# Performance work log

Measured on AMD Instinct MI355X. Metric: run time of the kernel, lower is better.

Reference implementation:

```python
import jax, jax.numpy as jnp
import numpy as np

MARGIN = 1.0
EPS = 1e-12


def setup_inputs() -> dict:
    key = jax.random.key(0)
    k1, k2, k3 = jax.random.split(key, 3)
    B, C, D = 16384, 500, 512
    features = jax.random.normal(k1, (B, D), dtype=jnp.float32)
    prototypes = jax.random.normal(k2, (C, D), dtype=jnp.float32)
    labels = jax.random.randint(k3, (B,), 0, C, dtype=jnp.int64)
    return {"features": features, "prototypes": prototypes, "labels": labels}


def reference(features, prototypes, labels):
    # Pairwise L2 distances [B, C] via the expanded form (no [B,C,D] intermediate)
    f2 = jnp.sum(features * features, axis=-1, keepdims=True)   # [B, 1]
    p2 = jnp.sum(prototypes * prototypes, axis=-1)               # [C]
    sq = f2 + p2 - 2.0 * (features @ prototypes.T)               # [B, C]
    dists = jnp.sqrt(jnp.maximum(sq, EPS))                       # [B, C]

    B, C = dists.shape
    d_pos = jnp.take_along_axis(dists, labels[:, None], axis=1)[:, 0]  # [B]
    pos_mask = jax.nn.one_hot(labels, C, dtype=bool)             # [B, C]
    d_neg_min = jnp.min(jnp.where(pos_mask, jnp.inf, dists), axis=-1)  # [B]

    loss = jnp.mean(jax.nn.relu(d_pos - d_neg_min + MARGIN))
    return loss
```

## Files before the change

### kernel.cpp

```cpp
#include <hip/hip_runtime.h>
#include <stdint.h>
#include <stddef.h>

#define BB 16384
#define CC 500
#define DD 512
#define PADC 512
#define LMARGIN 1.0f
#define EPSQ 1e-12f
#define NK 16

typedef __attribute__((ext_vector_type(8))) _Float16 f16x8;
typedef __attribute__((ext_vector_type(4))) _Float16 f16x4;
typedef __attribute__((ext_vector_type(4))) float f32x4;

__global__ void prepP_kernel(const float* __restrict__ protos,
                             unsigned short* __restrict__ protoH,
                             float* __restrict__ p2,
                             float* __restrict__ out) {
  int c = blockIdx.x * 4 + (threadIdx.x >> 6);
  int lane = threadIdx.x & 63;
  if (c == 0 && lane == 0) out[0] = 0.f;
  f32x4 a0 = {0.f, 0.f, 0.f, 0.f}, a1 = a0;
  if (c < CC) {
    const float* src = protos + (size_t)c * DD + lane * 8;
    a0 = *(const f32x4*)src;
    a1 = *(const f32x4*)(src + 4);
  }
  f16x8 h;
  float s = 0.f;
#pragma unroll
  for (int u = 0; u < 4; ++u) {
    h[u] = (_Float16)a0[u];
    h[u + 4] = (_Float16)a1[u];
    s = fmaf(a0[u], a0[u], s);
    s = fmaf(a1[u], a1[u], s);
  }
  *(f16x8*)(protoH + (size_t)c * DD + lane * 8) = h;
#pragma unroll
  for (int d = 1; d < 64; d <<= 1) s += __shfl_xor(s, d, 64);
  if (lane == 0) p2[c] = s;
}

__launch_bounds__(512, 2)
__global__ void main_kernel(const float* __restrict__ feat,
                            const unsigned short* __restrict__ protoH,
                            const float* __restrict__ p2,
                            const int* __restrict__ labels,
                            float* __restrict__ f2ws,
                            float2* __restrict__ ws2) {
  __shared__ __align__(16) unsigned short Afull[NK][64][32];

  const int tid = threadIdx.x;
  const int w = tid >> 6;
  const int lane = tid & 63;
  const int lane16 = lane & 15;
  const int quad = lane >> 4;
  const int r0 = blockIdx.x * 64;

  const unsigned short* pb = protoH + (size_t)(w * 64 + lane16) * DD + quad * 8;

  f16x8 bcur[4], bnxt[4];
#pragma unroll
  for (int nt = 0; nt < 4; ++nt) bcur[nt] = *(const f16x8*)(pb + nt * 16 * DD);

  {
    const f32x4* fsrc = (const f32x4*)(feat + (size_t)r0 * DD);
    f32x4 a[NK];
#pragma unroll
    for (int i = 0; i < NK; ++i) a[i] = fsrc[w * 1024 + i * 64 + lane];

    float f2row[8] = {0.f, 0.f, 0.f, 0.f, 0.f, 0.f, 0.f, 0.f};
#pragma unroll
    for (int i = 0; i < NK; ++i) {
      const int row = w * 8 + (i >> 1);
      const int k = (i & 1) * 256 + lane * 4;
      f16x4 h;
      float s = 0.f;
#pragma unroll
      for (int u = 0; u < 4; ++u) {
        h[u] = (_Float16)a[i][u];
        s = fmaf(a[i][u], a[i][u], s);
      }
      *(f16x4*)(&Afull[k >> 5][row][k & 31]) = h;
#pragma unroll
      for (int d = 1; d < 64; d <<= 1) s += __shfl_xor(s, d, 64);
      f2row[i >> 1] += s;
    }
    if (lane == 0) {
#pragma unroll
      for (int j = 0; j < 8; ++j) f2ws[r0 + w * 8 + j] = f2row[j];
    }
  }

  f32x4 acc[4][4];
#pragma unroll
  for (int mt = 0; mt < 4; ++mt)
#pragma unroll
    for (int nt = 0; nt < 4; ++nt) acc[mt][nt] = (f32x4){0.f, 0.f, 0.f, 0.f};

  __syncthreads();

#pragma unroll 2
  for (int kc = 0; kc < NK; ++kc) {
    if (kc + 1 < NK) {
#pragma unroll
      for (int nt = 0; nt < 4; ++nt)
        bnxt[nt] = *(const f16x8*)(pb + nt * 16 * DD + (kc + 1) * 32);
    }
    f16x8 af[4];
#pragma unroll
    for (int mt = 0; mt < 4; ++mt)
      af[mt] = *(const f16x8*)(&Afull[kc][mt * 16 + lane16][0] + quad * 8);
#pragma unroll
    for (int mt = 0; mt < 4; ++mt)
#pragma unroll
      for (int nt = 0; nt < 4; ++nt)
        acc[mt][nt] = __builtin_amdgcn_mfma_f32_16x16x32_f16(
            af[mt], bcur[nt], acc[mt][nt], 0, 0, 0);
#pragma unroll
    for (int nt = 0; nt < 4; ++nt) bcur[nt] = bnxt[nt];
  }

  float p2v[4];
#pragma unroll
  for (int nt = 0; nt < 4; ++nt) p2v[nt] = p2[w * 64 + nt * 16 + lane16];

#pragma unroll
  for (int mt = 0; mt < 4; ++mt) {
#pragma unroll
    for (int i = 0; i < 4; ++i) {
      const int row = mt * 16 + quad * 4 + i;
      const int lb = labels[r0 + row];
      float qm = 1e30f, qp = -1e30f;
#pragma unroll
      for (int nt = 0; nt < 4; ++nt) {
        const int col = w * 64 + nt * 16 + lane16;
        float q = p2v[nt] - 2.f * acc[mt][nt][i];
        bool isPos = (col == lb);
        qp = fmaxf(qp, isPos ? q : -1e30f);
        qm = fminf(qm, (!isPos && col < CC) ? q : 1e30f);
      }
#pragma unroll
      for (int d = 1; d < 16; d <<= 1) {
        qm = fminf(qm, __shfl_xor(qm, d, 64));
        qp = fmaxf(qp, __shfl_xor(qp, d, 64));
      }
      if (lane16 == 0) ws2[(size_t)(r0 + row) * 8 + w] = make_float2(qm, qp);
    }
  }
}

__global__ void reduce_kernel(const float2* __restrict__ ws2,
                              const float* __restrict__ f2ws,
                              float* __restrict__ out) {
  int row = blockIdx.x * 256 + threadIdx.x;
  const float4* v = (const float4*)ws2;
  float qm = 1e30f, qp = -1e30f;
#pragma unroll
  for (int j = 0; j < 4; ++j) {
    float4 a = v[(size_t)row * 4 + j];
    qm = fminf(qm, fminf(a.x, a.z));
    qp = fmaxf(qp, fmaxf(a.y, a.w));
  }
  float f2 = f2ws[row];
  float dn = sqrtf(fmaxf(f2 + qm, EPSQ));
  float dp = sqrtf(fmaxf(f2 + qp, EPSQ));
  float term = fmaxf(dp - dn + LMARGIN, 0.f);
#pragma unroll
  for (int d = 1; d < 64; d <<= 1) term += __shfl_xor(term, d, 64);
  __shared__ float ws4[4];
  if ((threadIdx.x & 63) == 0) ws4[threadIdx.x >> 6] = term;
  __syncthreads();
  if (threadIdx.x == 0)
    atomicAdd(out, (ws4[0] + ws4[1] + ws4[2] + ws4[3]) * (1.0f / BB));
}

extern "C" void kernel_launch(void* const* d_in, const int* in_sizes, int n_in,
                              void* d_out, int out_size, void* d_ws, size_t ws_size,
                              hipStream_t stream) {
  const float* feat = (const float*)d_in[0];
  const float* protos = (const float*)d_in[1];
  const int* labels = (const int*)d_in[2];
  float* out = (float*)d_out;

  char* ws = (char*)d_ws;
  unsigned short* protoH = (unsigned short*)(ws);
  float* p2 = (float*)(ws + (512 << 10));
  float* f2ws = (float*)(ws + (1 << 20));
  float2* ws2 = (float2*)(ws + (2 << 20));

  prepP_kernel<<<PADC / 4, 256, 0, stream>>>(protos, protoH, p2, out);
  main_kernel<<<BB / 64, 512, 0, stream>>>(feat, protoH, p2, labels, f2ws, ws2);
  reduce_kernel<<<BB / 256, 256, 0, stream>>>(ws2, f2ws, out);
}
```

Before: 101.7 us.

## Pipeline feature K-chunks through triple-buffered LDS and fuse final reduction

The main kernel now streams feature rows in K-chunks through a three-slot swizzled LDS ring buffer, so global loads of later chunks overlap with MFMA work instead of loading the whole tile up front. Prototypes are pre-tiled into an MFMA-fragment-friendly layout so each lane issues a contiguous 16-byte load, prefetched two chunks ahead. The per-row min/max combine, sqrt and hinge are done in-block with one atomic per block, which removes the separate reduce kernel and its workspace round-trip. The cost is a __syncthreads per K-chunk, higher register pressure from the prefetch buffers, and many atomics on a single output.

```diff
diff --git a/kernel.cpp b/kernel.cpp
--- a/kernel.cpp
+++ b/kernel.cpp
@@ -15,41 +15,55 @@
 typedef __attribute__((ext_vector_type(4))) float f32x4;
 
 __global__ void prepP_kernel(const float* __restrict__ protos,
-                             unsigned short* __restrict__ protoH,
+                             unsigned short* __restrict__ protoT,
                              float* __restrict__ p2,
                              float* __restrict__ out) {
-  int c = blockIdx.x * 4 + (threadIdx.x >> 6);
-  int lane = threadIdx.x & 63;
-  if (c == 0 && lane == 0) out[0] = 0.f;
-  f32x4 a0 = {0.f, 0.f, 0.f, 0.f}, a1 = a0;
-  if (c < CC) {
-    const float* src = protos + (size_t)c * DD + lane * 8;
-    a0 = *(const f32x4*)src;
-    a1 = *(const f32x4*)(src + 4);
-  }
-  f16x8 h;
+  __shared__ float s_arr[16][17];
+  const int cg = blockIdx.x;
+  const int t = threadIdx.x;
+  const int colin = t & 15;
+  const int jb = t >> 4;
+  const int col = cg * 16 + colin;
+  if (cg == 0 && t == 0) out[0] = 0.f;
   float s = 0.f;
 #pragma unroll
   for (int u = 0; u < 4; ++u) {
-    h[u] = (_Float16)a0[u];
-    h[u + 4] = (_Float16)a1[u];
-    s = fmaf(a0[u], a0[u], s);
-    s = fmaf(a1[u], a1[u], s);
-  }
-  *(f16x8*)(protoH + (size_t)c * DD + lane * 8) = h;
-#pragma unroll
-  for (int d = 1; d < 64; d <<= 1) s += __shfl_xor(s, d, 64);
-  if (lane == 0) p2[c] = s;
+    const int j8 = jb + u * 16;
+    const int kc = j8 >> 2, quad = j8 & 3;
+    f32x4 a0 = {0.f, 0.f, 0.f, 0.f}, a1 = a0;
+    if (col < CC) {
+      const float* src = protos + (size_t)col * DD + j8 * 8;
+      a0 = *(const f32x4*)src;
+      a1 = *(const f32x4*)(src + 4);
+    }
+    f16x8 h;
+#pragma unroll
+    for (int uu = 0; uu < 4; ++uu) {
+      h[uu] = (_Float16)a0[uu];
+      h[uu + 4] = (_Float16)a1[uu];
+      s = fmaf(a0[uu], a0[uu], s);
+      s = fmaf(a1[uu], a1[uu], s);
+    }
+    *(f16x8*)(protoT + (size_t)(cg * 16 + kc) * 512 + (quad * 16 + colin) * 8) = h;
+  }
+  s_arr[colin][jb] = s;
+  __syncthreads();
+  if (t < 16) {
+    float acc = 0.f;
+#pragma unroll
+    for (int i = 0; i < 16; ++i) acc += s_arr[t][i];
+    p2[cg * 16 + t] = acc;
+  }
 }
 
 __launch_bounds__(512, 2)
 __global__ void main_kernel(const float* __restrict__ feat,
-                            const unsigned short* __restrict__ protoH,
+                            const unsigned short* __restrict__ protoT,
                             const float* __restrict__ p2,
                             const int* __restrict__ labels,
-                            float* __restrict__ f2ws,
-                            float2* __restrict__ ws2) {
-  __shared__ __align__(16) unsigned short Afull[NK][64][32];
+                            float* __restrict__ out) {
+  __shared__ __align__(16) unsigned char Ab[3][4096];
+  __shared__ float f2l[64];
 
   const int tid = threadIdx.x;
   const int w = tid >> 6;
@@ -58,69 +72,90 @@
   const int quad = lane >> 4;
   const int r0 = blockIdx.x * 64;
 
-  const unsigned short* pb = protoH + (size_t)(w * 64 + lane16) * DD + quad * 8;
-
-  f16x8 bcur[4], bnxt[4];
-#pragma unroll
-  for (int nt = 0; nt < 4; ++nt) bcur[nt] = *(const f16x8*)(pb + nt * 16 * DD);
+  float* redM = (float*)&Ab[1][0];
+  float* redP = (float*)&Ab[1][2048];
+
+  const int arow = tid >> 3;
+  const int aj = tid & 7;
+  const float* aSrc = feat + (size_t)(r0 + arow) * DD + aj * 4;
+  const int awoff = arow * 64 + (((aj >> 1) ^ ((arow >> 1) & 3)) * 16) + (aj & 1) * 8;
+  const int aroff = lane16 * 64 + ((quad ^ ((lane16 >> 1) & 3)) * 16);
+
+  const char* bptr[4];
+#pragma unroll
+  for (int nt = 0; nt < 4; ++nt)
+    bptr[nt] = (const char*)protoT + (size_t)((w * 4 + nt) * 16) * 1024 + lane * 16;
+
+  f32x4 acc[4][4];
+#pragma unroll
+  for (int mt = 0; mt < 4; ++mt)
+#pragma unroll
+    for (int nt = 0; nt < 4; ++nt) acc[mt][nt] = (f32x4){0.f, 0.f, 0.f, 0.f};
+
+  float f2acc = 0.f;
+  f16x8 bfr[3][4];
+  f32x4 aC;
 
   {
-    const f32x4* fsrc = (const f32x4*)(feat + (size_t)r0 * DD);
-    f32x4 a[NK];
-#pragma unroll
-    for (int i = 0; i < NK; ++i) a[i] = fsrc[w * 1024 + i * 64 + lane];
-
-    float f2row[8] = {0.f, 0.f, 0.f, 0.f, 0.f, 0.f, 0.f, 0.f};
-#pragma unroll
-    for (int i = 0; i < NK; ++i) {
-      const int row = w * 8 + (i >> 1);
-      const int k = (i & 1) * 256 + lane * 4;
-      f16x4 h;
-      float s = 0.f;
-#pragma unroll
-      for (int u = 0; u < 4; ++u) {
-        h[u] = (_Float16)a[i][u];
-        s = fmaf(a[i][u], a[i][u], s);
-      }
-      *(f16x4*)(&Afull[k >> 5][row][k & 31]) = h;
-#pragma unroll
-      for (int d = 1; d < 64; d <<= 1) s += __shfl_xor(s, d, 64);
-      f2row[i >> 1] += s;
-    }
-    if (lane == 0) {
-#pragma unroll
-      for (int j = 0; j < 8; ++j) f2ws[r0 + w * 8 + j] = f2row[j];
-    }
-  }
-
-  f32x4 acc[4][4];
-#pragma unroll
-  for (int mt = 0; mt < 4; ++mt)
-#pragma unroll
-    for (int nt = 0; nt < 4; ++nt) acc[mt][nt] = (f32x4){0.f, 0.f, 0.f, 0.f};
-
+    f32x4 a0 = *(const f32x4*)(aSrc);
+    f32x4 a1 = *(const f32x4*)(aSrc + 32);
+    aC = *(const f32x4*)(aSrc + 64);
+#pragma unroll
+    for (int nt = 0; nt < 4; ++nt) {
+      bfr[0][nt] = *(const f16x8*)(bptr[nt]);
+      bfr[1][nt] = *(const f16x8*)(bptr[nt] + 1024);
+    }
+    f16x4 h0, h1;
+#pragma unroll
+    for (int u = 0; u < 4; ++u) {
+      h0[u] = (_Float16)a0[u];
+      h1[u] = (_Float16)a1[u];
+      f2acc = fmaf(a0[u], a0[u], f2acc);
+      f2acc = fmaf(a1[u], a1[u], f2acc);
+    }
+    *(f16x4*)(&Ab[0][awoff]) = h0;
+    *(f16x4*)(&Ab[1][awoff]) = h1;
+  }
   __syncthreads();
 
-#pragma unroll 2
+#pragma unroll
   for (int kc = 0; kc < NK; ++kc) {
-    if (kc + 1 < NK) {
+    f32x4 aN;
+    if (kc + 3 < NK) aN = *(const f32x4*)(aSrc + (kc + 3) * 32);
+    if (kc + 2 < NK) {
 #pragma unroll
       for (int nt = 0; nt < 4; ++nt)
-        bnxt[nt] = *(const f16x8*)(pb + nt * 16 * DD + (kc + 1) * 32);
-    }
+        bfr[(kc + 2) % 3][nt] = *(const f16x8*)(bptr[nt] + (kc + 2) * 1024);
+    }
+
     f16x8 af[4];
 #pragma unroll
     for (int mt = 0; mt < 4; ++mt)
-      af[mt] = *(const f16x8*)(&Afull[kc][mt * 16 + lane16][0] + quad * 8);
+      af[mt] = *(const f16x8*)(&Ab[kc % 3][mt * 1024 + aroff]);
 #pragma unroll
     for (int mt = 0; mt < 4; ++mt)
 #pragma unroll
       for (int nt = 0; nt < 4; ++nt)
         acc[mt][nt] = __builtin_amdgcn_mfma_f32_16x16x32_f16(
-            af[mt], bcur[nt], acc[mt][nt], 0, 0, 0);
-#pragma unroll
-    for (int nt = 0; nt < 4; ++nt) bcur[nt] = bnxt[nt];
-  }
+            af[mt], bfr[kc % 3][nt], acc[mt][nt], 0, 0, 0);
+
+    if (kc + 2 < NK) {
+      f16x4 h;
+#pragma unroll
+      for (int u = 0; u < 4; ++u) {
+        h[u] = (_Float16)aC[u];
+        f2acc = fmaf(aC[u], aC[u], f2acc);
+      }
+      *(f16x4*)(&Ab[(kc + 2) % 3][awoff]) = h;
+      aC = aN;
+    }
+    __syncthreads();
+  }
+
+  f2acc += __shfl_xor(f2acc, 1, 64);
+  f2acc += __shfl_xor(f2acc, 2, 64);
+  f2acc += __shfl_xor(f2acc, 4, 64);
+  if ((tid & 7) == 0) f2l[arow] = f2acc;
 
   float p2v[4];
 #pragma unroll
@@ -146,34 +181,29 @@
         qm = fminf(qm, __shfl_xor(qm, d, 64));
         qp = fmaxf(qp, __shfl_xor(qp, d, 64));
       }
-      if (lane16 == 0) ws2[(size_t)(r0 + row) * 8 + w] = make_float2(qm, qp);
-    }
-  }
-}
-
-__global__ void reduce_kernel(const float2* __restrict__ ws2,
-                              const float* __restrict__ f2ws,
-                              float* __restrict__ out) {
-  int row = blockIdx.x * 256 + threadIdx.x;
-  const float4* v = (const float4*)ws2;
-  float qm = 1e30f, qp = -1e30f;
-#pragma unroll
-  for (int j = 0; j < 4; ++j) {
-    float4 a = v[(size_t)row * 4 + j];
-    qm = fminf(qm, fminf(a.x, a.z));
-    qp = fmaxf(qp, fmaxf(a.y, a.w));
-  }
-  float f2 = f2ws[row];
-  float dn = sqrtf(fmaxf(f2 + qm, EPSQ));
-  float dp = sqrtf(fmaxf(f2 + qp, EPSQ));
-  float term = fmaxf(dp - dn + LMARGIN, 0.f);
-#pragma unroll
-  for (int d = 1; d < 64; d <<= 1) term += __shfl_xor(term, d, 64);
-  __shared__ float ws4[4];
-  if ((threadIdx.x & 63) == 0) ws4[threadIdx.x >> 6] = term;
+      if (lane16 == 0) {
+        redM[row * 8 + w] = qm;
+        redP[row * 8 + w] = qp;
+      }
+    }
+  }
   __syncthreads();
-  if (threadIdx.x == 0)
-    atomicAdd(out, (ws4[0] + ws4[1] + ws4[2] + ws4[3]) * (1.0f / BB));
+
+  if (tid < 64) {
+    float qm = 1e30f, qp = -1e30f;
+#pragma unroll
+    for (int j = 0; j < 8; ++j) {
+      qm = fminf(qm, redM[tid * 8 + j]);
+      qp = fmaxf(qp, redP[tid * 8 + j]);
+    }
+    float f2 = f2l[tid];
+    float dn = sqrtf(fmaxf(f2 + qm, EPSQ));
+    float dp = sqrtf(fmaxf(f2 + qp, EPSQ));
+    float term = fmaxf(dp - dn + LMARGIN, 0.f);
+#pragma unroll
+    for (int d = 1; d < 64; d <<= 1) term += __shfl_xor(term, d, 64);
+    if (tid == 0) atomicAdd(out, term * (1.0f / BB));
+  }
 }
 
 extern "C" void kernel_launch(void* const* d_in, const int* in_sizes, int n_in,
@@ -185,12 +215,9 @@
   float* out = (float*)d_out;
 
   char* ws = (char*)d_ws;
-  unsigned short* protoH = (unsigned short*)(ws);
+  unsigned short* protoT = (unsigned short*)(ws);
   float* p2 = (float*)(ws + (512 << 10));
-  float* f2ws = (float*)(ws + (1 << 20));
-  float2* ws2 = (float2*)(ws + (2 << 20));
-
-  prepP_kernel<<<PADC / 4, 256, 0, stream>>>(protos, protoH, p2, out);
-  main_kernel<<<BB / 64, 512, 0, stream>>>(feat, protoH, p2, labels, f2ws, ws2);
-  reduce_kernel<<<BB / 256, 256, 0, stream>>>(ws2, f2ws, out);
+
+  prepP_kernel<<<32, 256, 0, stream>>>(protos, protoT, p2, out);
+  main_kernel<<<BB / 64, 512, 0, stream>>>(feat, protoT, p2, labels, out);
 }
```

Result: faster. 93.62 us (-7.9%).
